# Kernel optimization log

Hardware: AMD Instinct MI355X
Metric: run time of the kernel (lower is better)

Reference implementation:

```python
import jax, jax.numpy as jnp
import numpy as np

DIM = 768
NUM_HEADS = 12
HEAD_DIM = DIM // NUM_HEADS
MAX_H = 32
MAX_W = 32


def setup_inputs() -> dict:
    key = jax.random.key(0)
    ks = jax.random.split(key, 7)
    B, H, W = 2, MAX_H, MAX_W
    N = H * W
    x = jax.random.normal(ks[0], (B, N, DIM), dtype=jnp.float32)
    qkv_w = jax.random.normal(ks[1], (3 * DIM, DIM), dtype=jnp.float32) * 0.02
    qkv_b = jax.random.normal(ks[2], (3 * DIM,), dtype=jnp.float32) * 0.02
    proj_w = jax.random.normal(ks[3], (DIM, DIM), dtype=jnp.float32) * 0.02
    proj_b = jax.random.normal(ks[4], (DIM,), dtype=jnp.float32) * 0.02
    rel_pos_h = jax.random.normal(ks[5], (2 * MAX_H - 1, HEAD_DIM), dtype=jnp.float32) * 0.02
    rel_pos_w = jax.random.normal(ks[6], (2 * MAX_W - 1, HEAD_DIM), dtype=jnp.float32) * 0.02
    return {"x": x, "qkv_w": qkv_w, "qkv_b": qkv_b, "proj_w": proj_w,
            "proj_b": proj_b, "rel_pos_h": rel_pos_h, "rel_pos_w": rel_pos_w,
            "x_h": H, "x_w": W}


def _rel_index(q_size, k_size):
    # q_size == k_size here (x_hw == max_hw), ratios are 1 and _interpolate is identity
    dist = jnp.arange(q_size)[:, None] - jnp.arange(k_size)[None, :] + (k_size - 1)
    return dist  # values in [0, 2*k_size-2]


def reference(x, qkv_w, qkv_b, proj_w, proj_b, rel_pos_h, rel_pos_w, x_h, x_w):
    B, N, dim = x.shape
    nh, hd = NUM_HEADS, HEAD_DIM
    qkv = (x @ qkv_w.T + qkv_b).reshape(B, N, 3, nh, hd)
    q, k, v = qkv[:, :, 0], qkv[:, :, 1], qkv[:, :, 2]  # [B, N, nh, hd]

    Rh = rel_pos_h[_rel_index(x_h, x_h)]  # [qh, kh, hd]
    Rw = rel_pos_w[_rel_index(x_w, x_w)]  # [qw, kw, hd]
    q2d = q.reshape(B, x_h, x_w, nh, hd)
    rel_h = jnp.einsum('bhwnc,hkc->bnhwk', q2d, Rh)  # [B, nh, qh, qw, kh]
    rel_w = jnp.einsum('bhwnc,wkc->bnhwk', q2d, Rw)  # [B, nh, qh, qw, kw]
    bias = (rel_h[..., :, None] + rel_w[..., None, :]).reshape(B, nh, N, N)

    scale = 1.0 / np.sqrt(hd).astype(np.float32)
    scores = jnp.einsum('bqhd,bkhd->bhqk', q, k) * scale + bias
    attn = jax.nn.softmax(scores, axis=-1)
    out = jnp.einsum('bhqk,bkhd->bqhd', attn, v).reshape(B, N, dim)
    return out @ proj_w.T + proj_b
```

## Files before the change

kernel.cpp:

```cpp
#include <hip/hip_runtime.h>

typedef float fx4 __attribute__((ext_vector_type(4)));
typedef float fx2 __attribute__((ext_vector_type(2)));
typedef short bfrag __attribute__((ext_vector_type(8)));
typedef float ffrag __attribute__((ext_vector_type(4)));
typedef unsigned short ush;

#define NTOK  1024
#define NHEADS 12
#define HD    64
#define DIMM  768

__device__ __forceinline__ float b2f(ush u) {
  union { unsigned i; float f; } x; x.i = ((unsigned)u) << 16; return x.f;
}
__device__ __forceinline__ ush f2b(float f) {
  union { float f; unsigned i; } x; x.f = f;
  unsigned r = x.i + 0x7fff + ((x.i >> 16) & 1);
  return (ush)(r >> 16);
}

__device__ __forceinline__ void gload16(const void* g, void* l) {
  __builtin_amdgcn_global_load_lds(
      (const __attribute__((address_space(1))) unsigned*)g,
      (__attribute__((address_space(3))) unsigned*)l, 16, 0, 0);
}

__device__ __forceinline__ ffrag mfma16(bfrag a, bfrag b, ffrag c) {
  return __builtin_amdgcn_mfma_f32_16x16x32_bf16(a, b, c, 0, 0, 0);
}

template<int N> __device__ __forceinline__ void vwait() {
  if constexpr (N == 0)       asm volatile("s_waitcnt vmcnt(0)" ::: "memory");
  else if constexpr (N == 4)  asm volatile("s_waitcnt vmcnt(4)" ::: "memory");
  else if constexpr (N == 6)  asm volatile("s_waitcnt vmcnt(6)" ::: "memory");
  else                        asm volatile("s_waitcnt vmcnt(8)" ::: "memory");
}
__device__ __forceinline__ void bar() {
  asm volatile("" ::: "memory");
  __builtin_amdgcn_s_barrier();
  asm volatile("" ::: "memory");
}
__device__ __forceinline__ void barL() {
  asm volatile("s_waitcnt lgkmcnt(0)" ::: "memory");
  __builtin_amdgcn_s_barrier();
  asm volatile("" ::: "memory");
}

__device__ __forceinline__ int swz(int row, int b) {
  return row * 128 + (b ^ ((row & 7) << 4));
}

__global__ __launch_bounds__(256) void k_cvt3(
    const float* __restrict__ x, const float* __restrict__ w,
    const float* __restrict__ pw, const float* __restrict__ rph,
    const float* __restrict__ rpw,
    ush* __restrict__ xh, ush* __restrict__ xl,
    ush* __restrict__ wh,
    ush* __restrict__ pwh, ush* __restrict__ pwl,
    ush* __restrict__ rphh, ush* __restrict__ rphl,
    ush* __restrict__ rpwh, ush* __restrict__ rpwl)
{
  int i = blockIdx.x * 256 + threadIdx.x;
  if (i >= 985056) return;
  const float* src; ush *h, *l; int off;
  bool lo = true;
  if (i < 393216)      { src = x;  h = xh;  l = xl;  off = i; }
  else if (i < 835584) { src = w;  h = wh;  l = nullptr; lo = false; off = i - 393216; }
  else if (i < 983040) { src = pw; h = pwh; l = pwl; off = i - 835584; }
  else if (i < 984048) { src = rph; h = rphh; l = rphl; off = i - 983040; }
  else                 { src = rpw; h = rpwh; l = rpwl; off = i - 984048; }
  fx4 v = *(const fx4*)(src + (size_t)off * 4);
  ushort4 hh, ll;
  float t;
  hh.x = f2b(v[0]); t = v[0] - b2f(hh.x); ll.x = f2b(t);
  hh.y = f2b(v[1]); t = v[1] - b2f(hh.y); ll.y = f2b(t);
  hh.z = f2b(v[2]); t = v[2] - b2f(hh.z); ll.z = f2b(t);
  hh.w = f2b(v[3]); t = v[3] - b2f(hh.w); ll.w = f2b(t);
  *(ushort4*)(h + (size_t)off * 4) = hh;
  if (lo) *(ushort4*)(l + (size_t)off * 4) = ll;
}

template<int MR, int NR, int NTERM>
__device__ __forceinline__ void gemm_pipe(
    const ush* __restrict__ Ah, const ush* __restrict__ Al,
    const ush* __restrict__ Bh, const ush* __restrict__ Bl,
    int row0, int col0, int K, short* lds, ffrag (&acc)[MR][NR])
{
  constexpr int F = (NTERM == 3) ? 4 * (MR + NR) : (4 * MR + 2 * NR);
  constexpr int LPS = F / 4;
  static_assert(F % 4 == 0, "frag count must be divisible by wave count");
  const int tid = threadIdx.x;
  const int lane = tid & 63, w = tid >> 6;
  const int wr = w >> 1, wc = w & 1;
  const int l15 = lane & 15, l8 = (lane >> 4) * 8;

  auto stage = [&](short* buf, int k0) {
    #pragma unroll
    for (int i = 0; i < LPS; i++) {
      int f = i * 4 + w;
      const ush* src;
      if (f < 2 * MR)
        src = Ah + (size_t)(row0 + f * 16 + l15) * K + k0 + l8;
      else if (f < 4 * MR)
        src = Al + (size_t)(row0 + (f - 2 * MR) * 16 + l15) * K + k0 + l8;
      else if (f < 4 * MR + 2 * NR)
        src = Bh + (size_t)(col0 + (f - 4 * MR) * 16 + l15) * K + k0 + l8;
      else
        src = Bl + (size_t)(col0 + (f - 4 * MR - 2 * NR) * 16 + l15) * K + k0 + l8;
      gload16(src, buf + f * 512);
    }
  };

  auto step = [&](const short* buf) {
    bfrag ah[MR], al[MR], bh[NR];
    #pragma unroll
    for (int i = 0; i < MR; i++) {
      ah[i] = *(const bfrag*)(buf + (wr * MR + i) * 512 + lane * 8);
      al[i] = *(const bfrag*)(buf + (2 * MR + wr * MR + i) * 512 + lane * 8);
    }
    #pragma unroll
    for (int j = 0; j < NR; j++)
      bh[j] = *(const bfrag*)(buf + (4 * MR + wc * NR + j) * 512 + lane * 8);
    if constexpr (NTERM == 3) {
      bfrag bl[NR];
      #pragma unroll
      for (int j = 0; j < NR; j++)
        bl[j] = *(const bfrag*)(buf + (4 * MR + 2 * NR + wc * NR + j) * 512 + lane * 8);
      #pragma unroll
      for (int i = 0; i < MR; i++)
        #pragma unroll
        for (int j = 0; j < NR; j++) {
          acc[i][j] = mfma16(ah[i], bh[j], acc[i][j]);
          acc[i][j] = mfma16(ah[i], bl[j], acc[i][j]);
          acc[i][j] = mfma16(al[i], bh[j], acc[i][j]);
        }
    } else {
      #pragma unroll
      for (int i = 0; i < MR; i++)
        #pragma unroll
        for (int j = 0; j < NR; j++) {
          acc[i][j] = mfma16(ah[i], bh[j], acc[i][j]);
          acc[i][j] = mfma16(al[i], bh[j], acc[i][j]);
        }
    }
  };

  const int nt = K / 32;
  stage(lds, 0);
  for (int t = 0; t < nt; t++) {
    bar();
    if (t + 1 < nt) {
      stage(lds + ((t + 1) & 1) * F * 512, (t + 1) * 32);
      vwait<LPS>();
    } else {
      vwait<0>();
    }
    bar();
    step(lds + (t & 1) * F * 512);
  }
}

__global__ __launch_bounds__(256) void k_qkv_mfma(
    const ush* __restrict__ xh, const ush* __restrict__ xl,
    const ush* __restrict__ wh,
    const float* __restrict__ bias,
    ush* __restrict__ qo, ush* __restrict__ ko, ush* __restrict__ vo)
{
  __shared__ short lds[2 * 24 * 512];
  const int orig = blockIdx.x;
  const int xcd = orig & 7, local = orig >> 3;
  const int lm = local & 3, ln = local >> 2;
  const int bm = (xcd & 3) * 4 + lm;
  const int bn = (xcd >> 2) * 9 + ln;
  const int row0 = bm * 128, col0 = bn * 128;
  ffrag acc[4][4] = {};
  gemm_pipe<4, 4, 2>(xh, xl, wh, wh, row0, col0, 768, lds, acc);

  const int tid = threadIdx.x, lane = tid & 63, w = tid >> 6;
  const int wr = w >> 1, wc = w & 1;
  const int l15 = lane & 15, l4 = lane >> 4;
  const int which = col0 / 768;
  const int base_head = (col0 - which * 768) >> 6;
  const int head = base_head + wc;
  ush* base = which == 0 ? qo : (which == 1 ? ko : vo);
  #pragma unroll
  for (int mi = 0; mi < 4; mi++)
    #pragma unroll
    for (int ni = 0; ni < 4; ni++) {
      int d = ni * 16 + l15;
      float bv = bias[col0 + wc * 64 + d];
      #pragma unroll
      for (int r = 0; r < 4; r++) {
        int row = row0 + wr * 64 + mi * 16 + l4 * 4 + r;
        int bb = row >> 10, n = row & 1023;
        base[((size_t)(bb * NHEADS + head) * NTOK + n) * HD + d] =
            f2b(acc[mi][ni][r] + bv);
      }
    }
}

__global__ __launch_bounds__(256) void k_proj_mfma(
    const ush* __restrict__ ah, const ush* __restrict__ al,
    const ush* __restrict__ bh, const ush* __restrict__ bl,
    const float* __restrict__ bias, float* __restrict__ out)
{
  __shared__ short lds[2 * 16 * 512];
  const int orig = blockIdx.x;
  const int xcd = orig & 7, local = orig >> 3;
  const int lm = local & 7, ln = local >> 3;
  const int bm = (xcd & 3) * 8 + lm;
  const int bn = (xcd >> 2) * 6 + ln;
  const int row0 = bm * 64, col0 = bn * 64;
  ffrag acc[2][2] = {};
  gemm_pipe<2, 2, 3>(ah, al, bh, bl, row0, col0, 768, lds, acc);

  const int tid = threadIdx.x, lane = tid & 63, w = tid >> 6;
  const int wr = w >> 1, wc = w & 1;
  const int l15 = lane & 15, l4 = lane >> 4;
  #pragma unroll
  for (int mi = 0; mi < 2; mi++)
    #pragma unroll
    for (int ni = 0; ni < 2; ni++) {
      int col = col0 + wc * 32 + ni * 16 + l15;
      float bv = bias[col];
      #pragma unroll
      for (int r = 0; r < 4; r++) {
        int row = row0 + wr * 32 + mi * 16 + l4 * 4 + r;
        out[(size_t)row * 768 + col] = acc[mi][ni][r] + bv;
      }
    }
}

__global__ __launch_bounds__(256, 3) void k_attn_mfma(
    const ush* __restrict__ qT, const ush* __restrict__ kT,
    const ush* __restrict__ vT,
    const ush* __restrict__ rphh, const ush* __restrict__ rphl,
    const ush* __restrict__ rpwh, const ush* __restrict__ rpwl,
    float* __restrict__ opf, float* __restrict__ ml)
{
  __shared__ short Kf[2 * 8 * 512];
  __shared__ char VTb[8192];
  __shared__ char Phb[8192];
  __shared__ char Plb[8192];
  __shared__ float RhS[64][34];

  const int orig = blockIdx.x;
  const int bid = (orig & 7) * 96 + (orig >> 3);
  const int ks   = bid & 1;
  const int qt   = (bid >> 1) & 15;
  const int pair = bid >> 5;
  const int q0 = qt * 64;
  const ush* qp = qT + (size_t)pair * NTOK * HD;
  const ush* kp = kT + (size_t)pair * NTOK * HD;
  const ush* vp = vT + (size_t)pair * NTOK * HD;

  const int tid = threadIdx.x;
  const int lane = tid & 63, w = tid >> 6;
  const int l15 = lane & 15, l4 = lane >> 4;
  const int wq = w * 16;
  const int kv = tid & 63, db = tid >> 6;

  auto issueK = [&](int tt) {
    const int gt = ks * 8 + tt;
    const ush* s0 = kp + (size_t)(gt * 64 + wq + l15) * HD + l4 * 8;
    short* dst = Kf + (tt & 1) * 4096 + (w * 2) * 512;
    gload16(s0, dst);
    gload16(s0 + 32, dst + 512);
  };
  auto issueV = [&](int tt, ushort4 (&vr)[4]) {
    const int gt = ks * 8 + tt;
    #pragma unroll
    for (int j = 0; j < 4; j++)
      vr[j] = *(const ushort4*)(vp + (size_t)(gt * 64 + kv) * HD + db * 16 + j * 4);
  };
  auto writeVT = [&](ushort4 (&vr)[4]) {
    #pragma unroll
    for (int j = 0; j < 4; j++) {
      int d0 = db * 16 + j * 4;
      *(ush*)(VTb + swz(d0 + 0, 2 * kv)) = vr[j].x;
      *(ush*)(VTb + swz(d0 + 1, 2 * kv)) = vr[j].y;
      *(ush*)(VTb + swz(d0 + 2, 2 * kv)) = vr[j].z;
      *(ush*)(VTb + swz(d0 + 3, 2 * kv)) = vr[j].w;
    }
  };

  bfrag qf[2];
  qf[0] = *(const bfrag*)(qp + (size_t)(q0 + wq + l15) * HD + l4 * 8);
  qf[1] = *(const bfrag*)(qp + (size_t)(q0 + wq + l15) * HD + 32 + l4 * 8);

  {
    const int qh = (q0 + wq) >> 5;
    #pragma unroll
    for (int kb = 0; kb < 2; kb++) {
      int rrow = qh + 31 - (kb * 16 + l15);
      const ush* bh = rphh + rrow * 64 + l4 * 8;
      const ush* bl = rphl + rrow * 64 + l4 * 8;
      bfrag b0 = *(const bfrag*)bh;
      bfrag b1 = *(const bfrag*)(bh + 32);
      bfrag c0 = *(const bfrag*)bl;
      bfrag c1 = *(const bfrag*)(bl + 32);
      ffrag s = {};
      s = mfma16(qf[0], b0, s);
      s = mfma16(qf[1], b1, s);
      s = mfma16(qf[0], c0, s);
      s = mfma16(qf[1], c1, s);
      #pragma unroll
      for (int r = 0; r < 4; r++)
        RhS[wq + l4 * 4 + r][kb * 16 + l15] = s[r];
    }
  }

  float rw[4][2];
  {
    #pragma unroll
    for (int dbk = 0; dbk < 4; dbk++) {
      int rrow = dbk * 16 + l15;
      const ush* bh = rpwh + rrow * 64 + l4 * 8;
      const ush* bl = rpwl + rrow * 64 + l4 * 8;
      bfrag b0 = *(const bfrag*)bh;
      bfrag b1 = *(const bfrag*)(bh + 32);
      bfrag c0 = *(const bfrag*)bl;
      bfrag c1 = *(const bfrag*)(bl + 32);
      ffrag s = {};
      s = mfma16(qf[0], b0, s);
      s = mfma16(qf[1], b1, s);
      s = mfma16(qf[0], c0, s);
      s = mfma16(qf[1], c1, s);
      #pragma unroll
      for (int r = 0; r < 4; r++) {
        int row = l4 * 4 + r, d = dbk * 16 + l15;
        float* dst = (d < 32)
          ? (float*)(Phb + (wq + row) * 128 + (d & 31) * 4)
          : (float*)(Plb + (wq + row) * 128 + (d & 31) * 4);
        *dst = s[r];
      }
    }
    #pragma unroll
    for (int r = 0; r < 4; r++) {
      int row = l4 * 4 + r;
      int qw = (q0 + wq + row) & 31;
      #pragma unroll
      for (int h = 0; h < 2; h++) {
        int d = qw + 31 - (h * 16 + l15);
        const float* srcp = (d < 32)
          ? (const float*)(Phb + (wq + row) * 128 + (d & 31) * 4)
          : (const float*)(Plb + (wq + row) * 128 + (d & 31) * 4);
        rw[r][h] = *srcp;
      }
    }
  }

  asm volatile("" ::: "memory");
  ushort4 vrA[4], vrB[4];
  issueK(0); issueV(0, vrA); issueV(1, vrB);

  ffrag o[4] = {};
  float mrow[4] = {-3e38f, -3e38f, -3e38f, -3e38f};
  float lrow[4] = {};

  for (int tt = 0; tt < 8; tt++) {
    const int t = ks * 8 + tt;
    if (tt < 7) vwait<4>(); else vwait<0>();
    barL();

    if ((tt & 1) == 0) {
      writeVT(vrA);
      if (tt < 7) issueK(tt + 1);
      if (tt < 6) issueV(tt + 2, vrA);
    } else {
      writeVT(vrB);
      if (tt < 7) issueK(tt + 1);
      if (tt < 6) issueV(tt + 2, vrB);
    }

    const short* kbuf = Kf + (tt & 1) * 4096;
    ffrag s[4] = {};
    #pragma unroll
    for (int kf = 0; kf < 4; kf++) {
      bfrag kf0 = *(const bfrag*)(kbuf + (kf * 2 + 0) * 512 + lane * 8);
      bfrag kf1 = *(const bfrag*)(kbuf + (kf * 2 + 1) * 512 + lane * 8);
      s[kf] = mfma16(qf[0], kf0, s[kf]);
      s[kf] = mfma16(qf[1], kf1, s[kf]);
    }

    fx2 rh2[4];
    #pragma unroll
    for (int r = 0; r < 4; r++)
      rh2[r] = *(const fx2*)&RhS[wq + l4 * 4 + r][2 * t];
    float pm[4] = {-3e38f, -3e38f, -3e38f, -3e38f};
    #pragma unroll
    for (int kf = 0; kf < 4; kf++)
      #pragma unroll
      for (int r = 0; r < 4; r++) {
        float sc = fmaf(s[kf][r], 0.125f, rh2[r][kf >> 1] + rw[r][kf & 1]);
        s[kf][r] = sc;
        pm[r] = fmaxf(pm[r], sc);
      }
    #pragma unroll
    for (int off = 1; off < 16; off <<= 1)
      #pragma unroll
      for (int r = 0; r < 4; r++)
        pm[r] = fmaxf(pm[r], __shfl_xor(pm[r], off));
    float al[4];
    #pragma unroll
    for (int r = 0; r < 4; r++) {
      float mnew = fmaxf(mrow[r], pm[r]);
      al[r] = __expf(mrow[r] - mnew);
      mrow[r] = mnew;
    }
    float ps[4] = {0.f, 0.f, 0.f, 0.f};
    #pragma unroll
    for (int kf = 0; kf < 4; kf++)
      #pragma unroll
      for (int r = 0; r < 4; r++) {
        float p = __expf(s[kf][r] - mrow[r]);
        s[kf][r] = p;
        ps[r] += p;
      }
    #pragma unroll
    for (int r = 0; r < 4; r++)
      lrow[r] = fmaf(lrow[r], al[r], ps[r]);

    #pragma unroll
    for (int kf = 0; kf < 4; kf++)
      #pragma unroll
      for (int rp = 0; rp < 2; rp++) {
        float s0 = s[kf][rp * 2], s1 = s[kf][rp * 2 + 1];
        unsigned hp;
        asm("v_cvt_pk_bf16_f32 %0, %1, %2" : "=v"(hp) : "v"(s0), "v"(s1));
        union { unsigned u; float f; } u0, u1;
        u0.u = hp << 16;
        u1.u = hp & 0xffff0000u;
        float l0 = s0 - u0.f, l1 = s1 - u1.f;
        unsigned lp;
        asm("v_cvt_pk_bf16_f32 %0, %1, %2" : "=v"(lp) : "v"(l0), "v"(l1));
        int a0 = swz(wq + l4 * 4 + rp * 2,     kf * 32 + 2 * l15);
        int a1 = swz(wq + l4 * 4 + rp * 2 + 1, kf * 32 + 2 * l15);
        *(ush*)(Phb + a0) = (ush)hp;
        *(ush*)(Phb + a1) = (ush)(hp >> 16);
        *(ush*)(Plb + a0) = (ush)lp;
        *(ush*)(Plb + a1) = (ush)(lp >> 16);
      }
    #pragma unroll
    for (int df = 0; df < 4; df++)
      #pragma unroll
      for (int r = 0; r < 4; r++)
        o[df][r] *= al[r];

    barL();

    bfrag ph[2], pl[2];
    #pragma unroll
    for (int kc = 0; kc < 2; kc++) {
      int a = swz(wq + l15, kc * 64 + l4 * 16);
      ph[kc] = *(const bfrag*)(Phb + a);
      pl[kc] = *(const bfrag*)(Plb + a);
    }
    #pragma unroll
    for (int df = 0; df < 4; df++)
      #pragma unroll
      for (int kc = 0; kc < 2; kc++) {
        bfrag vf = *(const bfrag*)(VTb + swz(df * 16 + l15, kc * 64 + l4 * 16));
        o[df] = mfma16(ph[kc], vf, o[df]);
        o[df] = mfma16(pl[kc], vf, o[df]);
      }
  }

  #pragma unroll
  for (int off = 1; off < 16; off <<= 1)
    #pragma unroll
    for (int r = 0; r < 4; r++)
      lrow[r] += __shfl_xor(lrow[r], off);

  const int part = ((pair << 4) | qt) * 2 + ks;
  if (l15 == 0) {
    float* mlp = ml + (size_t)part * 128;
    #pragma unroll
    for (int r = 0; r < 4; r++) {
      int row = wq + l4 * 4 + r;
      mlp[row] = mrow[r];
      mlp[64 + row] = lrow[r];
    }
  }
  float* obase = opf + (size_t)part * 4096;
  #pragma unroll
  for (int df = 0; df < 4; df++)
    #pragma unroll
    for (int r = 0; r < 4; r++) {
      int row = wq + l4 * 4 + r;
      obase[(size_t)row * 64 + df * 16 + l15] = o[df][r];
    }
}

__global__ __launch_bounds__(256) void k_attn_merge(
    const float* __restrict__ opf, const float* __restrict__ ml,
    ush* __restrict__ o1h, ush* __restrict__ o1l)
{
  const int pq = blockIdx.x;
  const int pair = pq >> 4, qt = pq & 15;
  const int bb = pair / NHEADS, head = pair % NHEADS;
  __shared__ float M0[64], L0[64], M1[64], L1[64];
  const int tid = threadIdx.x;
  const float* mlp = ml + (size_t)pq * 256;
  if (tid < 64) {
    M0[tid] = mlp[tid];        L0[tid] = mlp[64 + tid];
    M1[tid] = mlp[128 + tid];  L1[tid] = mlp[192 + tid];
  }
  __syncthreads();
  const float* b0 = opf + (size_t)(pq * 2) * 4096;
  const float* b1 = b0 + 4096;
  #pragma unroll
  for (int e = 0; e < 4; e++) {
    int q4 = e * 256 + tid;
    int row = q4 >> 4;
    int d4 = (q4 & 15) * 4;
    float m0 = M0[row], l0v = L0[row], m1 = M1[row], l1v = L1[row];
    float m = fmaxf(m0, m1);
    float a0 = __expf(m0 - m), a1 = __expf(m1 - m);
    float inv = 1.0f / (l0v * a0 + l1v * a1);
    fx4 v0 = *(const fx4*)(b0 + (size_t)q4 * 4);
    fx4 v1 = *(const fx4*)(b1 + (size_t)q4 * 4);
    float r0 = (v0[0] * a0 + v1[0] * a1) * inv;
    float r1 = (v0[1] * a0 + v1[1] * a1) * inv;
    float r2 = (v0[2] * a0 + v1[2] * a1) * inv;
    float r3 = (v0[3] * a0 + v1[3] * a1) * inv;
    size_t gidx = ((size_t)(bb * NTOK + qt * 64 + row)) * DIMM + head * HD + d4;
    ushort4 oh, ol;
    oh.x = f2b(r0); ol.x = f2b(r0 - b2f(oh.x));
    oh.y = f2b(r1); ol.y = f2b(r1 - b2f(oh.y));
    oh.z = f2b(r2); ol.z = f2b(r2 - b2f(oh.z));
    oh.w = f2b(r3); ol.w = f2b(r3 - b2f(oh.w));
    *(ushort4*)(o1h + gidx) = oh;
    *(ushort4*)(o1l + gidx) = ol;
  }
}

extern "C" void kernel_launch(void* const* d_in, const int* in_sizes, int n_in,
                              void* d_out, int out_size, void* d_ws, size_t ws_size,
                              hipStream_t stream)
{
  const float* x      = (const float*)d_in[0];
  const float* qkv_w  = (const float*)d_in[1];
  const float* qkv_b  = (const float*)d_in[2];
  const float* proj_w = (const float*)d_in[3];
  const float* proj_b = (const float*)d_in[4];
  const float* rph    = (const float*)d_in[5];
  const float* rpw    = (const float*)d_in[6];

  char* p = (char*)d_ws;
  ush* xh  = (ush*)p; p += 3145728;
  ush* xl  = (ush*)p; p += 3145728;
  ush* wh  = (ush*)p; p += 3538944;
  ush* wl  = (ush*)p; p += 3538944;
  ush* pwh = (ush*)p; p += 1179648;
  ush* pwl = (ush*)p; p += 1179648;
  ush* qb  = (ush*)p; p += 3145728;
  ush* kb  = (ush*)p; p += 3145728;
  ush* vb  = (ush*)p; p += 3145728;
  float* ml = (float*)p; p += 393216;
  ush* rphh = (ush*)p; p += 8192;
  ush* rphl = (ush*)p; p += 8192;
  ush* rpwh = (ush*)p; p += 8192;
  ush* rpwl = (ush*)p; p += 8192;
  (void)wl;
  float* opf = (float*)xh;
  ush* o1h = qb;
  ush* o1l = kb;
  float* out = (float*)d_out;

  k_cvt3<<<dim3(3849), dim3(256), 0, stream>>>(x, qkv_w, proj_w, rph, rpw,
                                               xh, xl, wh, pwh, pwl,
                                               rphh, rphl, rpwh, rpwl);
  k_qkv_mfma<<<dim3(288), dim3(256), 0, stream>>>(xh, xl, wh, qkv_b, qb, kb, vb);
  k_attn_mfma<<<dim3(768), dim3(256), 0, stream>>>(qb, kb, vb,
                                                   rphh, rphl, rpwh, rpwl,
                                                   opf, ml);
  k_attn_merge<<<dim3(384), dim3(256), 0, stream>>>(opf, ml, o1h, o1l);
  k_proj_mfma<<<dim3(384), dim3(256), 0, stream>>>(o1h, o1l, pwh, pwl, proj_b, out);
}
```

Measured before the change: 119.3 us.

## Drop P low-part split, double-buffer V tile, remove second barrier per KV tile

The attention kernel no longer splits the softmax probabilities into bf16 high and low parts. It stores a single bf16 P, which halves the PV MFMAs and the LDS writes for P. The V-transpose buffer is double-buffered, reusing the freed Plb space, so the V write can happen before the single per-iteration barrier and the second barrier is removed. This lowers the precision of the P·V product and relies on each wave reading only its own rows of Phb so that the removed barrier is safe.

```diff
diff --git a/kernel.cpp b/kernel.cpp
--- a/kernel.cpp
+++ b/kernel.cpp
@@ -240,9 +240,8 @@
     float* __restrict__ opf, float* __restrict__ ml)
 {
   __shared__ short Kf[2 * 8 * 512];
-  __shared__ char VTb[8192];
-  __shared__ char Phb[8192];
-  __shared__ char Plb[8192];
+  __shared__ __align__(16) char VTb[2][8192];
+  __shared__ __align__(16) char Phb[8192];
   __shared__ float RhS[64][34];
 
   const int orig = blockIdx.x;
@@ -274,14 +273,15 @@
     for (int j = 0; j < 4; j++)
       vr[j] = *(const ushort4*)(vp + (size_t)(gt * 64 + kv) * HD + db * 16 + j * 4);
   };
-  auto writeVT = [&](ushort4 (&vr)[4]) {
+  auto writeVT = [&](int buf, ushort4 (&vr)[4]) {
+    char* base = VTb[buf];
     #pragma unroll
     for (int j = 0; j < 4; j++) {
       int d0 = db * 16 + j * 4;
-      *(ush*)(VTb + swz(d0 + 0, 2 * kv)) = vr[j].x;
-      *(ush*)(VTb + swz(d0 + 1, 2 * kv)) = vr[j].y;
-      *(ush*)(VTb + swz(d0 + 2, 2 * kv)) = vr[j].z;
-      *(ush*)(VTb + swz(d0 + 3, 2 * kv)) = vr[j].w;
+      *(ush*)(base + swz(d0 + 0, 2 * kv)) = vr[j].x;
+      *(ush*)(base + swz(d0 + 1, 2 * kv)) = vr[j].y;
+      *(ush*)(base + swz(d0 + 2, 2 * kv)) = vr[j].z;
+      *(ush*)(base + swz(d0 + 3, 2 * kv)) = vr[j].w;
     }
   };
 
@@ -332,7 +332,7 @@
         int row = l4 * 4 + r, d = dbk * 16 + l15;
         float* dst = (d < 32)
           ? (float*)(Phb + (wq + row) * 128 + (d & 31) * 4)
-          : (float*)(Plb + (wq + row) * 128 + (d & 31) * 4);
+          : (float*)(VTb[0] + (wq + row) * 128 + (d & 31) * 4);
         *dst = s[r];
       }
     }
@@ -345,13 +345,13 @@
         int d = qw + 31 - (h * 16 + l15);
         const float* srcp = (d < 32)
           ? (const float*)(Phb + (wq + row) * 128 + (d & 31) * 4)
-          : (const float*)(Plb + (wq + row) * 128 + (d & 31) * 4);
+          : (const float*)(VTb[0] + (wq + row) * 128 + (d & 31) * 4);
         rw[r][h] = *srcp;
       }
     }
   }
-
-  asm volatile("" ::: "memory");
+  barL();
+
   ushort4 vrA[4], vrB[4];
   issueK(0); issueV(0, vrA); issueV(1, vrB);
 
@@ -362,16 +362,14 @@
   for (int tt = 0; tt < 8; tt++) {
     const int t = ks * 8 + tt;
     if (tt < 7) vwait<4>(); else vwait<0>();
+
+    if ((tt & 1) == 0) writeVT(0, vrA); else writeVT(1, vrB);
+
     barL();
 
-    if ((tt & 1) == 0) {
-      writeVT(vrA);
-      if (tt < 7) issueK(tt + 1);
-      if (tt < 6) issueV(tt + 2, vrA);
-    } else {
-      writeVT(vrB);
-      if (tt < 7) issueK(tt + 1);
-      if (tt < 6) issueV(tt + 2, vrB);
+    if (tt + 1 < 8) issueK(tt + 1);
+    if (tt + 2 < 8) {
+      if ((tt & 1) == 0) issueV(tt + 2, vrA); else issueV(tt + 2, vrB);
     }
 
     const short* kbuf = Kf + (tt & 1) * 4096;
@@ -429,18 +427,10 @@
         float s0 = s[kf][rp * 2], s1 = s[kf][rp * 2 + 1];
         unsigned hp;
         asm("v_cvt_pk_bf16_f32 %0, %1, %2" : "=v"(hp) : "v"(s0), "v"(s1));
-        union { unsigned u; float f; } u0, u1;
-        u0.u = hp << 16;
-        u1.u = hp & 0xffff0000u;
-        float l0 = s0 - u0.f, l1 = s1 - u1.f;
-        unsigned lp;
-        asm("v_cvt_pk_bf16_f32 %0, %1, %2" : "=v"(lp) : "v"(l0), "v"(l1));
         int a0 = swz(wq + l4 * 4 + rp * 2,     kf * 32 + 2 * l15);
         int a1 = swz(wq + l4 * 4 + rp * 2 + 1, kf * 32 + 2 * l15);
         *(ush*)(Phb + a0) = (ush)hp;
         *(ush*)(Phb + a1) = (ush)(hp >> 16);
-        *(ush*)(Plb + a0) = (ush)lp;
-        *(ush*)(Plb + a1) = (ush)(lp >> 16);
       }
     #pragma unroll
     for (int df = 0; df < 4; df++)
@@ -448,22 +438,19 @@
       for (int r = 0; r < 4; r++)
         o[df][r] *= al[r];
 
-    barL();
-
-    bfrag ph[2], pl[2];
+    const char* vtb = VTb[tt & 1];
+    bfrag ph[2];
     #pragma unroll
     for (int kc = 0; kc < 2; kc++) {
       int a = swz(wq + l15, kc * 64 + l4 * 16);
       ph[kc] = *(const bfrag*)(Phb + a);
-      pl[kc] = *(const bfrag*)(Plb + a);
     }
     #pragma unroll
     for (int df = 0; df < 4; df++)
       #pragma unroll
       for (int kc = 0; kc < 2; kc++) {
-        bfrag vf = *(const bfrag*)(VTb + swz(df * 16 + l15, kc * 64 + l4 * 16));
+        bfrag vf = *(const bfrag*)(vtb + swz(df * 16 + l15, kc * 64 + l4 * 16));
         o[df] = mfma16(ph[kc], vf, o[df]);
-        o[df] = mfma16(pl[kc], vf, o[df]);
       }
   }
 
```

Result: faster. 116.3 us (-2.5%).
